# Performance work log

Hardware: AMD Instinct MI355X
Metric: run time of the kernel (lower is better)

Reference implementation:

```python
import jax, jax.numpy as jnp
import numpy as np

B, T, C = 4, 2048, 768
N_HEAD = 12
HEAD_DIM = C // N_HEAD


def setup_inputs() -> dict:
    key = jax.random.key(0)
    ks = jax.random.split(key, 9)
    s = 1.0 / np.sqrt(C)
    return {
        "x": jax.random.normal(ks[0], (B, T, C), dtype=jnp.float32),
        "Wq": jax.random.normal(ks[1], (C, C), dtype=jnp.float32) * s,
        "bq": jnp.zeros((C,), dtype=jnp.float32),
        "Wk": jax.random.normal(ks[2], (C, C), dtype=jnp.float32) * s,
        "bk": jnp.zeros((C,), dtype=jnp.float32),
        "Wv": jax.random.normal(ks[3], (C, C), dtype=jnp.float32) * s,
        "bv": jnp.zeros((C,), dtype=jnp.float32),
        "Wo": jax.random.normal(ks[4], (C, C), dtype=jnp.float32) * s,
        "bo": jnp.zeros((C,), dtype=jnp.float32),
    }


def reference(x, Wq, bq, Wk, bk, Wv, bv, Wo, bo):
    Bx, Tx, Cx = x.shape
    q = x @ Wq + bq  # [B,T,C]
    k = x @ Wk + bk
    v = x @ Wv + bv
    # [B,H,T,hd]
    q = q.reshape(Bx, Tx, N_HEAD, HEAD_DIM).transpose(0, 2, 1, 3)
    k = k.reshape(Bx, Tx, N_HEAD, HEAD_DIM).transpose(0, 2, 1, 3)
    v = v.reshape(Bx, Tx, N_HEAD, HEAD_DIM).transpose(0, 2, 1, 3)
    scale = 1.0 / np.sqrt(HEAD_DIM).astype(np.float32)
    att = jnp.einsum('bhqd,bhkd->bhqk', q, k) * scale  # [B,H,T,T]
    causal = jnp.tril(jnp.ones((Tx, Tx), dtype=bool))
    att = jnp.where(causal[None, None], att, jnp.float32(-jnp.inf))
    att = jax.nn.softmax(att, axis=-1)
    # dropout p=0.0 -> identity
    y = jnp.einsum('bhqk,bhkd->bhqd', att, v)  # [B,H,T,hd]
    y = y.transpose(0, 2, 1, 3).reshape(Bx, Tx, Cx)
    return y @ Wo + bo
```

## Files before the change

kernel.cpp:

```cpp
#include <hip/hip_runtime.h>

#define T_DIM 2048
#define C_DIM 768
#define NH    12
#define HD    64
#define M_TOK 8192
#define PSTR2 72

typedef unsigned short ushort_t;
typedef __attribute__((ext_vector_type(8))) __bf16 bf16x8;
typedef __attribute__((ext_vector_type(4))) float  f32x4;

#define QSCALE 0.18033688011112042f

__device__ __forceinline__ unsigned short f32_to_bf16(float f) {
    unsigned u = __builtin_bit_cast(unsigned, f);
    u += 0x7FFFu + ((u >> 16) & 1u);
    return (unsigned short)(u >> 16);
}

__device__ __forceinline__ unsigned cvt_pk_bf16(float a, float b) {
    unsigned r;
    asm("v_cvt_pk_bf16_f32 %0, %1, %2" : "=v"(r) : "v"(a), "v"(b));
    return r;
}

__device__ __forceinline__ float fast_exp2(float x) {
#if __has_builtin(__builtin_amdgcn_exp2f)
    return __builtin_amdgcn_exp2f(x);
#else
    return exp2f(x);
#endif
}

__device__ __forceinline__ void gload_lds16(const void* g, void* l) {
    __builtin_amdgcn_global_load_lds(
        (const __attribute__((address_space(1))) unsigned int*)g,
        (__attribute__((address_space(3))) unsigned int*)l, 16, 0, 0);
}


__global__ void cvt_x_kernel(const float* __restrict__ in, ushort_t* __restrict__ out, int n4) {
    int i = blockIdx.x * blockDim.x + threadIdx.x;
    if (i >= n4) return;
    float4 v = ((const float4*)in)[i];
    ushort4 o;
    o.x = f32_to_bf16(v.x); o.y = f32_to_bf16(v.y);
    o.z = f32_to_bf16(v.z); o.w = f32_to_bf16(v.w);
    ((ushort4*)out)[i] = o;
}

__global__ void cvt_wT_tiled(
    const float* __restrict__ w0, const float* __restrict__ w1,
    const float* __restrict__ w2, const float* __restrict__ w3,
    ushort_t* __restrict__ t0, ushort_t* __restrict__ t1,
    ushort_t* __restrict__ t2, ushort_t* __restrict__ t3)
{
    __shared__ float tile[32][33];
    const int wsel = blockIdx.z;
    const float* w = (wsel == 0) ? w0 : (wsel == 1) ? w1 : (wsel == 2) ? w2 : w3;
    ushort_t* wT   = (wsel == 0) ? t0 : (wsel == 1) ? t1 : (wsel == 2) ? t2 : t3;
    const int n0 = blockIdx.x * 32, k0 = blockIdx.y * 32;
    const int tx = threadIdx.x & 31, ty = threadIdx.x >> 5;
    #pragma unroll
    for (int r = 0; r < 32; r += 8)
        tile[ty + r][tx] = w[(size_t)(k0 + ty + r) * C_DIM + n0 + tx];
    __syncthreads();
    #pragma unroll
    for (int r = 0; r < 32; r += 8)
        wT[(size_t)(n0 + ty + r) * C_DIM + k0 + tx] = f32_to_bf16(tile[tx][ty + r]);
}

__global__ void transpose_v(const ushort_t* __restrict__ vrow, ushort_t* __restrict__ vT) {
    __shared__ ushort_t tile[32][33];
    const int bh = blockIdx.z;
    const int t0 = blockIdx.x * 32, d0 = blockIdx.y * 32;
    const int tx = threadIdx.x & 31, ty = threadIdx.x >> 5;
    const ushort_t* src = vrow + (size_t)bh * T_DIM * HD;
    ushort_t* dst = vT + (size_t)bh * HD * T_DIM;
    #pragma unroll
    for (int r = 0; r < 32; r += 8)
        tile[ty + r][tx] = src[(size_t)(t0 + ty + r) * HD + d0 + tx];
    __syncthreads();
    #pragma unroll
    for (int r = 0; r < 32; r += 8)
        dst[(size_t)(d0 + ty + r) * T_DIM + t0 + tx] = tile[tx][ty + r];
}

__global__ __launch_bounds__(256) void qkv_gemm(
    const ushort_t* __restrict__ xbf,
    const ushort_t* __restrict__ wqT, const ushort_t* __restrict__ wkT, const ushort_t* __restrict__ wvT,
    const float* __restrict__ bq, const float* __restrict__ bk, const float* __restrict__ bv,
    ushort_t* __restrict__ qout, ushort_t* __restrict__ kout, ushort_t* __restrict__ vout)
{
    __shared__ ushort_t Alds[128 * 32];
    __shared__ ushort_t Blds[128 * 32];
    const int tid  = threadIdx.x;
    const int lane = tid & 63;
    const int wid  = tid >> 6;
    const int wr = wid >> 1, wc = wid & 1;
    const int lr = lane & 15, lk = lane >> 4;
    const int m0 = blockIdx.x * 128;
    const int gy = blockIdx.y;
    const int wsel = gy / 6;
    const int n0 = (gy % 6) * 128;
    const ushort_t* WT   = (wsel == 0) ? wqT : (wsel == 1 ? wkT : wvT);
    const float*    bias = (wsel == 0) ? bq  : (wsel == 1 ? bk  : bv);

    f32x4 acc[4][4];
    const f32x4 z4 = {0.f, 0.f, 0.f, 0.f};
    #pragma unroll
    for (int m = 0; m < 4; ++m)
        #pragma unroll
        for (int n = 0; n < 4; ++n) acc[m][n] = z4;

    const ushort_t* Ag = xbf + (size_t)m0 * C_DIM;
    const ushort_t* Bg = WT  + (size_t)n0 * C_DIM;

    for (int kb = 0; kb < C_DIM; kb += 32) {
        #pragma unroll
        for (int r = 0; r < 2; ++r) {
            int c = r * 256 + tid;
            int row = c >> 2;
            int co  = (c & 3) * 8;
            gload_lds16(Ag + (size_t)row * C_DIM + kb + co, &Alds[c * 8]);
            gload_lds16(Bg + (size_t)row * C_DIM + kb + co, &Blds[c * 8]);
        }
        __syncthreads();
        bf16x8 a[4], b[4];
        #pragma unroll
        for (int m = 0; m < 4; ++m)
            a[m] = *(const bf16x8*)&Alds[(wr * 64 + m * 16 + lr) * 32 + lk * 8];
        #pragma unroll
        for (int n = 0; n < 4; ++n)
            b[n] = *(const bf16x8*)&Blds[(wc * 64 + n * 16 + lr) * 32 + lk * 8];
        #pragma unroll
        for (int m = 0; m < 4; ++m)
            #pragma unroll
            for (int n = 0; n < 4; ++n)
                acc[m][n] = __builtin_amdgcn_mfma_f32_16x16x32_bf16(a[m], b[n], acc[m][n], 0, 0, 0);
        __syncthreads();
    }

    #pragma unroll
    for (int n = 0; n < 4; ++n) {
        const int col = n0 + wc * 64 + n * 16 + lr;
        const float bv_ = bias[col];
        const int h = col >> 6, d = col & 63;
        #pragma unroll
        for (int m = 0; m < 4; ++m) {
            #pragma unroll
            for (int j = 0; j < 4; ++j) {
                const int row = m0 + wr * 64 + m * 16 + lk * 4 + j;
                const int bb = row >> 11, t = row & 2047;
                const float val = acc[m][n][j] + bv_;
                const size_t idx = ((size_t)(bb * NH + h) * T_DIM + t) * HD + d;
                if (wsel == 0)      qout[idx] = f32_to_bf16(val * QSCALE);
                else if (wsel == 1) kout[idx] = f32_to_bf16(val);
                else                vout[idx] = f32_to_bf16(val);
            }
        }
    }
}

__global__ __launch_bounds__(256, 3) void attn_kernel(
    const ushort_t* __restrict__ qg, const ushort_t* __restrict__ kg,
    const ushort_t* __restrict__ vTg, ushort_t* __restrict__ y)
{
    __shared__ ushort_t Klds[2][64 * 64];
    __shared__ ushort_t Vlds[2][64 * 64];
    __shared__ ushort_t Plds[4][2][16 * PSTR2];
    const int tid  = threadIdx.x;
    const int lane = tid & 63, wid = tid >> 6;
    const int lr = lane & 15, lk = lane >> 4;
    const int r7 = lr & 7;

    const int bid = blockIdx.x;
    const int qb  = (T_DIM / 128 - 1) - (bid / (4 * NH));
    const int bh  = bid % (4 * NH);
    const int bb = bh / NH, h = bh % NH;
    const int q0b = qb * 128;
    const int q0w = q0b + wid * 32;

    const ushort_t* Q = qg  + (size_t)bh * T_DIM * HD;
    const ushort_t* K = kg  + (size_t)bh * T_DIM * HD;
    const ushort_t* V = vTg + (size_t)bh * HD * T_DIM;
    ushort_t* plA = &Plds[wid][0][0];
    ushort_t* plB = &Plds[wid][1][0];

    int koff[2], voff[2], ldsoff[2];
    #pragma unroll
    for (int i = 0; i < 2; ++i) {
        const int row = (wid * 2 + i) * 8 + (lane >> 3);
        const int c16 = (lane & 7) ^ (row & 7);
        koff[i]   = row * HD + c16 * 8;
        voff[i]   = row * T_DIM + c16 * 8;
        ldsoff[i] = (wid * 2 + i) * 512 + lane * 8;
    }

    const bf16x8 qa0A = *(const bf16x8*)&Q[(size_t)(q0w + lr) * HD + lk * 8];
    const bf16x8 qa1A = *(const bf16x8*)&Q[(size_t)(q0w + lr) * HD + 32 + lk * 8];
    const bf16x8 qa0B = *(const bf16x8*)&Q[(size_t)(q0w + 16 + lr) * HD + lk * 8];
    const bf16x8 qa1B = *(const bf16x8*)&Q[(size_t)(q0w + 16 + lr) * HD + 32 + lk * 8];

    const f32x4 z4 = {0.f, 0.f, 0.f, 0.f};
    f32x4 accA[4], accB[4];
    #pragma unroll
    for (int n = 0; n < 4; ++n) { accA[n] = z4; accB[n] = z4; }
    float lAs = 0.f, lBs = 0.f;

    const int nitb  = q0b / 64 + 2;
    const int nfull = (q0w >= 63) ? ((q0w - 63) >> 6) + 1 : 0;
    const int nitw  = (q0w + 95) >> 6;

    #pragma unroll
    for (int i = 0; i < 2; ++i) {
        gload_lds16(K + koff[i], &Klds[0][ldsoff[i]]);
        gload_lds16(V + voff[i], &Vlds[0][ldsoff[i]]);
    }
    __syncthreads();

    for (int it = 0; it < nitb; ++it) {
        const int cur = it & 1;
        const int kv  = it * 64;
        if (it + 1 < nitb) {
            const int kvn = kv + 64;
            #pragma unroll
            for (int i = 0; i < 2; ++i) {
                gload_lds16(K + (size_t)kvn * HD + koff[i], &Klds[cur ^ 1][ldsoff[i]]);
                gload_lds16(V + kvn + voff[i], &Vlds[cur ^ 1][ldsoff[i]]);
            }
        }
        if (it < nfull) {
            #pragma unroll
            for (int t = 0; t < 4; ++t) {
                const int row = t * 16 + lr;
                const bf16x8 kb0 = *(const bf16x8*)&Klds[cur][row * 64 + ((lk ^ r7) * 8)];
                const bf16x8 kb1 = *(const bf16x8*)&Klds[cur][row * 64 + (((4 + lk) ^ r7) * 8)];
                f32x4 sA = __builtin_amdgcn_mfma_f32_16x16x32_bf16(kb0, qa0A, z4, 0, 0, 0);
                sA = __builtin_amdgcn_mfma_f32_16x16x32_bf16(kb1, qa1A, sA, 0, 0, 0);
                f32x4 sB = __builtin_amdgcn_mfma_f32_16x16x32_bf16(kb0, qa0B, z4, 0, 0, 0);
                sB = __builtin_amdgcn_mfma_f32_16x16x32_bf16(kb1, qa1B, sB, 0, 0, 0);
                const float pA0 = fast_exp2(sA[0]), pA1 = fast_exp2(sA[1]);
                const float pA2 = fast_exp2(sA[2]), pA3 = fast_exp2(sA[3]);
                lAs += (pA0 + pA1) + (pA2 + pA3);
                const float pB0 = fast_exp2(sB[0]), pB1 = fast_exp2(sB[1]);
                const float pB2 = fast_exp2(sB[2]), pB3 = fast_exp2(sB[3]);
                lBs += (pB0 + pB1) + (pB2 + pB3);
                const int poff = lr * PSTR2 + t * 16 + lk * 4;
                *(uint2*)&plA[poff] = make_uint2(cvt_pk_bf16(pA0, pA1), cvt_pk_bf16(pA2, pA3));
                *(uint2*)&plB[poff] = make_uint2(cvt_pk_bf16(pB0, pB1), cvt_pk_bf16(pB2, pB3));
            }
            __builtin_amdgcn_s_setprio(1);
            #pragma unroll
            for (int c = 0; c < 2; ++c) {
                const bf16x8 paA = *(const bf16x8*)&plA[lr * PSTR2 + c * 32 + lk * 8];
                const bf16x8 paB = *(const bf16x8*)&plB[lr * PSTR2 + c * 32 + lk * 8];
                #pragma unroll
                for (int n = 0; n < 4; ++n) {
                    const bf16x8 vb = *(const bf16x8*)&Vlds[cur][(n * 16 + lr) * 64 + (((c * 4 + lk) ^ r7) * 8)];
                    accA[n] = __builtin_amdgcn_mfma_f32_16x16x32_bf16(paA, vb, accA[n], 0, 0, 0);
                    accB[n] = __builtin_amdgcn_mfma_f32_16x16x32_bf16(paB, vb, accB[n], 0, 0, 0);
                }
            }
            __builtin_amdgcn_s_setprio(0);
        } else if (it < nitw) {
            #pragma unroll
            for (int t = 0; t < 4; ++t) {
                const int tk = kv + t * 16;
                const int poff = lr * PSTR2 + t * 16 + lk * 4;
                if (tk <= q0w + 31) {
                    const int row = t * 16 + lr;
                    const bf16x8 kb0 = *(const bf16x8*)&Klds[cur][row * 64 + ((lk ^ r7) * 8)];
                    const bf16x8 kb1 = *(const bf16x8*)&Klds[cur][row * 64 + (((4 + lk) ^ r7) * 8)];
                    f32x4 sA = __builtin_amdgcn_mfma_f32_16x16x32_bf16(kb0, qa0A, z4, 0, 0, 0);
                    sA = __builtin_amdgcn_mfma_f32_16x16x32_bf16(kb1, qa1A, sA, 0, 0, 0);
                    f32x4 sB = __builtin_amdgcn_mfma_f32_16x16x32_bf16(kb0, qa0B, z4, 0, 0, 0);
                    sB = __builtin_amdgcn_mfma_f32_16x16x32_bf16(kb1, qa1B, sB, 0, 0, 0);
                    const int kvc = tk + lk * 4;
                    const int rA = q0w + lr;
                    float aA0 = sA[0], aA1 = sA[1], aA2 = sA[2], aA3 = sA[3];
                    if (kvc + 0 > rA) aA0 = -1e30f;
                    if (kvc + 1 > rA) aA1 = -1e30f;
                    if (kvc + 2 > rA) aA2 = -1e30f;
                    if (kvc + 3 > rA) aA3 = -1e30f;
                    const float pA0 = fast_exp2(aA0), pA1 = fast_exp2(aA1);
                    const float pA2 = fast_exp2(aA2), pA3 = fast_exp2(aA3);
                    lAs += (pA0 + pA1) + (pA2 + pA3);
                    float aB0 = sB[0], aB1 = sB[1], aB2 = sB[2], aB3 = sB[3];
                    if (kvc + 0 > rA + 16) aB0 = -1e30f;
                    if (kvc + 1 > rA + 16) aB1 = -1e30f;
                    if (kvc + 2 > rA + 16) aB2 = -1e30f;
                    if (kvc + 3 > rA + 16) aB3 = -1e30f;
                    const float pB0 = fast_exp2(aB0), pB1 = fast_exp2(aB1);
                    const float pB2 = fast_exp2(aB2), pB3 = fast_exp2(aB3);
                    lBs += (pB0 + pB1) + (pB2 + pB3);
                    *(uint2*)&plA[poff] = make_uint2(cvt_pk_bf16(pA0, pA1), cvt_pk_bf16(pA2, pA3));
                    *(uint2*)&plB[poff] = make_uint2(cvt_pk_bf16(pB0, pB1), cvt_pk_bf16(pB2, pB3));
                } else {
                    *(uint2*)&plA[poff] = make_uint2(0u, 0u);
                    *(uint2*)&plB[poff] = make_uint2(0u, 0u);
                }
            }
            __builtin_amdgcn_s_setprio(1);
            #pragma unroll
            for (int c = 0; c < 2; ++c) {
                if (kv + c * 32 <= q0w + 31) {
                    const bf16x8 paA = *(const bf16x8*)&plA[lr * PSTR2 + c * 32 + lk * 8];
                    const bf16x8 paB = *(const bf16x8*)&plB[lr * PSTR2 + c * 32 + lk * 8];
                    #pragma unroll
                    for (int n = 0; n < 4; ++n) {
                        const bf16x8 vb = *(const bf16x8*)&Vlds[cur][(n * 16 + lr) * 64 + (((c * 4 + lk) ^ r7) * 8)];
                        accA[n] = __builtin_amdgcn_mfma_f32_16x16x32_bf16(paA, vb, accA[n], 0, 0, 0);
                        accB[n] = __builtin_amdgcn_mfma_f32_16x16x32_bf16(paB, vb, accB[n], 0, 0, 0);
                    }
                }
            }
            __builtin_amdgcn_s_setprio(0);
        }
        __syncthreads();
    }

    float la = lAs, lb = lBs;
    la += __shfl_xor(la, 16); la += __shfl_xor(la, 32);
    lb += __shfl_xor(lb, 16); lb += __shfl_xor(lb, 32);
    float lrA[4], lrB[4];
    #pragma unroll
    for (int j = 0; j < 4; ++j) {
        lrA[j] = __builtin_amdgcn_rcpf(__shfl(la, lk * 4 + j));
        lrB[j] = __builtin_amdgcn_rcpf(__shfl(lb, lk * 4 + j));
    }

    #pragma unroll
    for (int n = 0; n < 4; ++n) {
        #pragma unroll
        for (int j = 0; j < 4; ++j) {
            const int tA = q0w + lk * 4 + j;
            y[((size_t)bb * T_DIM + tA) * C_DIM + h * HD + n * 16 + lr] = f32_to_bf16(accA[n][j] * lrA[j]);
            const int tB = q0w + 16 + lk * 4 + j;
            y[((size_t)bb * T_DIM + tB) * C_DIM + h * HD + n * 16 + lr] = f32_to_bf16(accB[n][j] * lrB[j]);
        }
    }
}

__global__ __launch_bounds__(256) void out_gemm(
    const ushort_t* __restrict__ ybf, const ushort_t* __restrict__ woT,
    const float* __restrict__ bo, float* __restrict__ out)
{
    __shared__ ushort_t Alds[128 * 32];
    __shared__ ushort_t Blds[128 * 32];
    const int tid  = threadIdx.x;
    const int lane = tid & 63;
    const int wid  = tid >> 6;
    const int wr = wid >> 1, wc = wid & 1;
    const int lr = lane & 15, lk = lane >> 4;
    const int m0 = blockIdx.x * 128;
    const int n0 = blockIdx.y * 128;

    f32x4 acc[4][4];
    const f32x4 z4 = {0.f, 0.f, 0.f, 0.f};
    #pragma unroll
    for (int m = 0; m < 4; ++m)
        #pragma unroll
        for (int n = 0; n < 4; ++n) acc[m][n] = z4;

    const ushort_t* Ag = ybf + (size_t)m0 * C_DIM;
    const ushort_t* Bg = woT + (size_t)n0 * C_DIM;

    for (int kb = 0; kb < C_DIM; kb += 32) {
        #pragma unroll
        for (int r = 0; r < 2; ++r) {
            int c = r * 256 + tid;
            int row = c >> 2;
            int co  = (c & 3) * 8;
            gload_lds16(Ag + (size_t)row * C_DIM + kb + co, &Alds[c * 8]);
            gload_lds16(Bg + (size_t)row * C_DIM + kb + co, &Blds[c * 8]);
        }
        __syncthreads();
        bf16x8 a[4], b[4];
        #pragma unroll
        for (int m = 0; m < 4; ++m)
            a[m] = *(const bf16x8*)&Alds[(wr * 64 + m * 16 + lr) * 32 + lk * 8];
        #pragma unroll
        for (int n = 0; n < 4; ++n)
            b[n] = *(const bf16x8*)&Blds[(wc * 64 + n * 16 + lr) * 32 + lk * 8];
        #pragma unroll
        for (int m = 0; m < 4; ++m)
            #pragma unroll
            for (int n = 0; n < 4; ++n)
                acc[m][n] = __builtin_amdgcn_mfma_f32_16x16x32_bf16(a[m], b[n], acc[m][n], 0, 0, 0);
        __syncthreads();
    }

    #pragma unroll
    for (int n = 0; n < 4; ++n) {
        const int col = n0 + wc * 64 + n * 16 + lr;
        const float bv_ = bo[col];
        #pragma unroll
        for (int m = 0; m < 4; ++m) {
            #pragma unroll
            for (int j = 0; j < 4; ++j) {
                const int row = m0 + wr * 64 + m * 16 + lk * 4 + j;
                out[(size_t)row * C_DIM + col] = acc[m][n][j] + bv_;
            }
        }
    }
}


extern "C" void kernel_launch(void* const* d_in, const int* in_sizes, int n_in,
                              void* d_out, int out_size, void* d_ws, size_t ws_size,
                              hipStream_t stream)
{
    (void)in_sizes; (void)n_in; (void)out_size; (void)ws_size;
    const float* x  = (const float*)d_in[0];
    const float* Wq = (const float*)d_in[1];
    const float* bq = (const float*)d_in[2];
    const float* Wk = (const float*)d_in[3];
    const float* bk = (const float*)d_in[4];
    const float* Wv = (const float*)d_in[5];
    const float* bv = (const float*)d_in[6];
    const float* Wo = (const float*)d_in[7];
    const float* bo = (const float*)d_in[8];
    float* out = (float*)d_out;

    char* ws = (char*)d_ws;
    const size_t xbytes = (size_t)M_TOK * C_DIM * 2;
    const size_t wbytes = (size_t)C_DIM * C_DIM * 2;
    ushort_t* xbf  = (ushort_t*)(ws);
    ushort_t* wqT  = (ushort_t*)(ws + xbytes);
    ushort_t* wkT  = (ushort_t*)(ws + xbytes + 1 * wbytes);
    ushort_t* wvT  = (ushort_t*)(ws + xbytes + 2 * wbytes);
    ushort_t* woT  = (ushort_t*)(ws + xbytes + 3 * wbytes);
    ushort_t* qbf  = (ushort_t*)(ws + xbytes + 4 * wbytes);
    ushort_t* kbf  = (ushort_t*)(ws + 2 * xbytes + 4 * wbytes);
    ushort_t* vTbf = (ushort_t*)(ws + 3 * xbytes + 4 * wbytes);
    ushort_t* ybf  = xbf;
    ushort_t* vrow = (ushort_t*)d_out;

    const int n4 = (int)((size_t)M_TOK * C_DIM / 4);
    cvt_x_kernel<<<n4 / 256, 256, 0, stream>>>(x, xbf, n4);
    dim3 gt(C_DIM / 32, C_DIM / 32, 4);
    cvt_wT_tiled<<<gt, 256, 0, stream>>>(Wq, Wk, Wv, Wo, wqT, wkT, wvT, woT);
    dim3 g1(M_TOK / 128, 18);
    qkv_gemm<<<g1, 256, 0, stream>>>(xbf, wqT, wkT, wvT, bq, bk, bv, qbf, kbf, vrow);
    dim3 gv(T_DIM / 32, HD / 32, 4 * NH);
    transpose_v<<<gv, 256, 0, stream>>>(vrow, vTbf);
    attn_kernel<<<(T_DIM / 128) * 4 * NH, 256, 0, stream>>>(qbf, kbf, vTbf, ybf);
    dim3 g3(M_TOK / 128, C_DIM / 128);
    out_gemm<<<g3, 256, 0, stream>>>(ybf, woT, bo, out);
}
```

Before: 211.8 us.

## Fuse conversions, write V transposed from QKV GEMM, swizzle GEMM LDS

Merges the x conversion and weight transpose kernels into a single launch. The V transpose kernel is removed: the QKV GEMM epilogue now stages each wave's tile in shared memory and writes Q/K as vectorized rows and V directly in transposed layout. Both GEMMs XOR-swizzle the LDS chunk index to reduce bank conflicts on fragment reads. The cost is extra shared memory in qkv_gemm, which may lower occupancy, and some strided LDS reads in the V epilogue.

After: 208.8 us. No clear change (-1.4%).

```diff
diff --git a/kernel.cpp b/kernel.cpp
--- a/kernel.cpp
+++ b/kernel.cpp
@@ -6,6 +6,7 @@
 #define HD    64
 #define M_TOK 8192
 #define PSTR2 72
+#define ESTR  72
 
 typedef unsigned short ushort_t;
 typedef __attribute__((ext_vector_type(8))) __bf16 bf16x8;
@@ -39,28 +40,30 @@
         (__attribute__((address_space(3))) unsigned int*)l, 16, 0, 0);
 }
 
-
-__global__ void cvt_x_kernel(const float* __restrict__ in, ushort_t* __restrict__ out, int n4) {
-    int i = blockIdx.x * blockDim.x + threadIdx.x;
-    if (i >= n4) return;
-    float4 v = ((const float4*)in)[i];
-    ushort4 o;
-    o.x = f32_to_bf16(v.x); o.y = f32_to_bf16(v.y);
-    o.z = f32_to_bf16(v.z); o.w = f32_to_bf16(v.w);
-    ((ushort4*)out)[i] = o;
-}
-
-__global__ void cvt_wT_tiled(
+__global__ void fused_cvt(
+    const float* __restrict__ x, ushort_t* __restrict__ xout,
     const float* __restrict__ w0, const float* __restrict__ w1,
     const float* __restrict__ w2, const float* __restrict__ w3,
     ushort_t* __restrict__ t0, ushort_t* __restrict__ t1,
     ushort_t* __restrict__ t2, ushort_t* __restrict__ t3)
 {
     __shared__ float tile[32][33];
-    const int wsel = blockIdx.z;
+    const int bid = blockIdx.x;
+    if (bid < 6144) {
+        const int i = bid * 256 + threadIdx.x;
+        float4 v = ((const float4*)x)[i];
+        ushort4 o;
+        o.x = f32_to_bf16(v.x); o.y = f32_to_bf16(v.y);
+        o.z = f32_to_bf16(v.z); o.w = f32_to_bf16(v.w);
+        ((ushort4*)xout)[i] = o;
+        return;
+    }
+    const int wz = bid - 6144;
+    const int wsel = wz / 576;
+    const int tl = wz % 576;
     const float* w = (wsel == 0) ? w0 : (wsel == 1) ? w1 : (wsel == 2) ? w2 : w3;
     ushort_t* wT   = (wsel == 0) ? t0 : (wsel == 1) ? t1 : (wsel == 2) ? t2 : t3;
-    const int n0 = blockIdx.x * 32, k0 = blockIdx.y * 32;
+    const int n0 = (tl % 24) * 32, k0 = (tl / 24) * 32;
     const int tx = threadIdx.x & 31, ty = threadIdx.x >> 5;
     #pragma unroll
     for (int r = 0; r < 32; r += 8)
@@ -69,32 +72,17 @@
     #pragma unroll
     for (int r = 0; r < 32; r += 8)
         wT[(size_t)(n0 + ty + r) * C_DIM + k0 + tx] = f32_to_bf16(tile[tx][ty + r]);
-}
-
-__global__ void transpose_v(const ushort_t* __restrict__ vrow, ushort_t* __restrict__ vT) {
-    __shared__ ushort_t tile[32][33];
-    const int bh = blockIdx.z;
-    const int t0 = blockIdx.x * 32, d0 = blockIdx.y * 32;
-    const int tx = threadIdx.x & 31, ty = threadIdx.x >> 5;
-    const ushort_t* src = vrow + (size_t)bh * T_DIM * HD;
-    ushort_t* dst = vT + (size_t)bh * HD * T_DIM;
-    #pragma unroll
-    for (int r = 0; r < 32; r += 8)
-        tile[ty + r][tx] = src[(size_t)(t0 + ty + r) * HD + d0 + tx];
-    __syncthreads();
-    #pragma unroll
-    for (int r = 0; r < 32; r += 8)
-        dst[(size_t)(d0 + ty + r) * T_DIM + t0 + tx] = tile[tx][ty + r];
 }
 
 __global__ __launch_bounds__(256) void qkv_gemm(
     const ushort_t* __restrict__ xbf,
     const ushort_t* __restrict__ wqT, const ushort_t* __restrict__ wkT, const ushort_t* __restrict__ wvT,
     const float* __restrict__ bq, const float* __restrict__ bk, const float* __restrict__ bv,
-    ushort_t* __restrict__ qout, ushort_t* __restrict__ kout, ushort_t* __restrict__ vout)
+    ushort_t* __restrict__ qout, ushort_t* __restrict__ kout, ushort_t* __restrict__ vTout)
 {
     __shared__ ushort_t Alds[128 * 32];
     __shared__ ushort_t Blds[128 * 32];
+    __shared__ ushort_t Elds[4][64 * ESTR];
     const int tid  = threadIdx.x;
     const int lane = tid & 63;
     const int wid  = tid >> 6;
@@ -116,13 +104,14 @@
 
     const ushort_t* Ag = xbf + (size_t)m0 * C_DIM;
     const ushort_t* Bg = WT  + (size_t)n0 * C_DIM;
+    const int rsl = (lr >> 1) & 3;
 
     for (int kb = 0; kb < C_DIM; kb += 32) {
         #pragma unroll
         for (int r = 0; r < 2; ++r) {
             int c = r * 256 + tid;
             int row = c >> 2;
-            int co  = (c & 3) * 8;
+            int co  = ((c & 3) ^ ((row >> 1) & 3)) * 8;
             gload_lds16(Ag + (size_t)row * C_DIM + kb + co, &Alds[c * 8]);
             gload_lds16(Bg + (size_t)row * C_DIM + kb + co, &Blds[c * 8]);
         }
@@ -130,10 +119,10 @@
         bf16x8 a[4], b[4];
         #pragma unroll
         for (int m = 0; m < 4; ++m)
-            a[m] = *(const bf16x8*)&Alds[(wr * 64 + m * 16 + lr) * 32 + lk * 8];
+            a[m] = *(const bf16x8*)&Alds[(wr * 64 + m * 16 + lr) * 32 + (lk ^ rsl) * 8];
         #pragma unroll
         for (int n = 0; n < 4; ++n)
-            b[n] = *(const bf16x8*)&Blds[(wc * 64 + n * 16 + lr) * 32 + lk * 8];
+            b[n] = *(const bf16x8*)&Blds[(wc * 64 + n * 16 + lr) * 32 + (lk ^ rsl) * 8];
         #pragma unroll
         for (int m = 0; m < 4; ++m)
             #pragma unroll
@@ -142,23 +131,52 @@
         __syncthreads();
     }
 
-    #pragma unroll
-    for (int n = 0; n < 4; ++n) {
-        const int col = n0 + wc * 64 + n * 16 + lr;
-        const float bv_ = bias[col];
-        const int h = col >> 6, d = col & 63;
+    const int hcol = (n0 + wc * 64) >> 6;
+    const int tg0  = m0 + wr * 64;
+    ushort_t* el = &Elds[wid][0];
+    if (wsel != 2) {
+        ushort_t* outp = (wsel == 0) ? qout : kout;
+        const float scal = (wsel == 0) ? QSCALE : 1.0f;
         #pragma unroll
         for (int m = 0; m < 4; ++m) {
             #pragma unroll
-            for (int j = 0; j < 4; ++j) {
-                const int row = m0 + wr * 64 + m * 16 + lk * 4 + j;
-                const int bb = row >> 11, t = row & 2047;
-                const float val = acc[m][n][j] + bv_;
-                const size_t idx = ((size_t)(bb * NH + h) * T_DIM + t) * HD + d;
-                if (wsel == 0)      qout[idx] = f32_to_bf16(val * QSCALE);
-                else if (wsel == 1) kout[idx] = f32_to_bf16(val);
-                else                vout[idx] = f32_to_bf16(val);
-            }
+            for (int n = 0; n < 4; ++n) {
+                const float bv_ = bias[n0 + wc * 64 + n * 16 + lr];
+                #pragma unroll
+                for (int j = 0; j < 4; ++j)
+                    el[(lk * 4 + j) * ESTR + n * 16 + lr] =
+                        f32_to_bf16((acc[m][n][j] + bv_) * scal);
+            }
+            #pragma unroll
+            for (int p = 0; p < 4; ++p) {
+                const int rloc = p * 4 + lk;
+                const ushort4 v = *(const ushort4*)&el[rloc * ESTR + lr * 4];
+                const int tg = tg0 + m * 16 + rloc;
+                const int bb = tg >> 11, t = tg & 2047;
+                *(ushort4*)&outp[((size_t)(bb * NH + hcol) * T_DIM + t) * HD + lr * 4] = v;
+            }
+        }
+    } else {
+        #pragma unroll
+        for (int m = 0; m < 4; ++m)
+            #pragma unroll
+            for (int n = 0; n < 4; ++n) {
+                const float bv_ = bias[n0 + wc * 64 + n * 16 + lr];
+                #pragma unroll
+                for (int j = 0; j < 4; ++j)
+                    el[(m * 16 + lk * 4 + j) * ESTR + n * 16 + lr] =
+                        f32_to_bf16(acc[m][n][j] + bv_);
+            }
+        const int bb = tg0 >> 11, t0v = tg0 & 2047;
+        #pragma unroll
+        for (int p = 0; p < 16; ++p) {
+            const int dloc = p * 4 + lk;
+            ushort4 v;
+            v.x = el[(lr * 4 + 0) * ESTR + dloc];
+            v.y = el[(lr * 4 + 1) * ESTR + dloc];
+            v.z = el[(lr * 4 + 2) * ESTR + dloc];
+            v.w = el[(lr * 4 + 3) * ESTR + dloc];
+            *(ushort4*)&vTout[((size_t)(bb * NH + hcol) * HD + dloc) * T_DIM + t0v + lr * 4] = v;
         }
     }
 }
@@ -366,13 +384,14 @@
 
     const ushort_t* Ag = ybf + (size_t)m0 * C_DIM;
     const ushort_t* Bg = woT + (size_t)n0 * C_DIM;
+    const int rsl = (lr >> 1) & 3;
 
     for (int kb = 0; kb < C_DIM; kb += 32) {
         #pragma unroll
         for (int r = 0; r < 2; ++r) {
             int c = r * 256 + tid;
             int row = c >> 2;
-            int co  = (c & 3) * 8;
+            int co  = ((c & 3) ^ ((row >> 1) & 3)) * 8;
             gload_lds16(Ag + (size_t)row * C_DIM + kb + co, &Alds[c * 8]);
             gload_lds16(Bg + (size_t)row * C_DIM + kb + co, &Blds[c * 8]);
         }
@@ -380,10 +399,10 @@
         bf16x8 a[4], b[4];
         #pragma unroll
         for (int m = 0; m < 4; ++m)
-            a[m] = *(const bf16x8*)&Alds[(wr * 64 + m * 16 + lr) * 32 + lk * 8];
+            a[m] = *(const bf16x8*)&Alds[(wr * 64 + m * 16 + lr) * 32 + (lk ^ rsl) * 8];
         #pragma unroll
         for (int n = 0; n < 4; ++n)
-            b[n] = *(const bf16x8*)&Blds[(wc * 64 + n * 16 + lr) * 32 + lk * 8];
+            b[n] = *(const bf16x8*)&Blds[(wc * 64 + n * 16 + lr) * 32 + (lk ^ rsl) * 8];
         #pragma unroll
         for (int m = 0; m < 4; ++m)
             #pragma unroll
@@ -436,16 +455,10 @@
     ushort_t* kbf  = (ushort_t*)(ws + 2 * xbytes + 4 * wbytes);
     ushort_t* vTbf = (ushort_t*)(ws + 3 * xbytes + 4 * wbytes);
     ushort_t* ybf  = xbf;
-    ushort_t* vrow = (ushort_t*)d_out;
-
-    const int n4 = (int)((size_t)M_TOK * C_DIM / 4);
-    cvt_x_kernel<<<n4 / 256, 256, 0, stream>>>(x, xbf, n4);
-    dim3 gt(C_DIM / 32, C_DIM / 32, 4);
-    cvt_wT_tiled<<<gt, 256, 0, stream>>>(Wq, Wk, Wv, Wo, wqT, wkT, wvT, woT);
+
+    fused_cvt<<<6144 + 2304, 256, 0, stream>>>(x, xbf, Wq, Wk, Wv, Wo, wqT, wkT, wvT, woT);
     dim3 g1(M_TOK / 128, 18);
-    qkv_gemm<<<g1, 256, 0, stream>>>(xbf, wqT, wkT, wvT, bq, bk, bv, qbf, kbf, vrow);
-    dim3 gv(T_DIM / 32, HD / 32, 4 * NH);
-    transpose_v<<<gv, 256, 0, stream>>>(vrow, vTbf);
+    qkv_gemm<<<g1, 256, 0, stream>>>(xbf, wqT, wkT, wvT, bq, bk, bv, qbf, kbf, vTbf);
     attn_kernel<<<(T_DIM / 128) * 4 * NH, 256, 0, stream>>>(qbf, kbf, vTbf, ybf);
     dim3 g3(M_TOK / 128, C_DIM / 128);
     out_gemm<<<g3, 256, 0, stream>>>(ybf, woT, bo, out);
```
